# Kernel optimization log

Hardware: AMD Instinct MI355X
Metric: run time of the kernel (lower is better)

Reference implementation:

```python
import jax, jax.numpy as jnp
import numpy as np

BANDWIDTH = 1.0


def setup_inputs() -> dict:
    key = jax.random.key(0)
    k1, k2 = jax.random.split(key)
    test_data = jax.random.normal(k1, (8192, 512), dtype=jnp.float32)
    train_data = jax.random.normal(k2, (16384, 512), dtype=jnp.float32)
    return {"test_data": test_data, "train_data": train_data}


def reference(test_data, train_data):
    # test_data: [N, D], train_data: [M, D]
    bw = jnp.asarray(BANDWIDTH, dtype=test_data.dtype)
    n_train, d = train_data.shape
    # (avoids materializing the [N, M, D] difference tensor)
    x2 = jnp.sum(test_data * test_data, axis=-1, keepdims=True)        # [N, 1]
    y2 = jnp.sum(train_data * train_data, axis=-1)[None, :]           # [1, M]
    xy = jnp.einsum('nd,md->nm', test_data, train_data)               # [N, M]
    sq_dist = jnp.maximum(x2 + y2 - 2.0 * xy, 0.0)                    # [N, M]
    log_exp = -0.5 * sq_dist / (bw * bw)
    # normalization constant z = 0.5*d*log(2*pi) + d*log(bw) + log(n)
    z = (0.5 * d * jnp.log(jnp.asarray(2.0 * np.pi, dtype=test_data.dtype))
         + d * jnp.log(bw)
         + jnp.log(jnp.asarray(float(n_train), dtype=test_data.dtype)))
    return jax.scipy.special.logsumexp(log_exp - z, axis=-1)          # [N]
```

## Files before the change

kernel.cpp:

```cpp
#include <hip/hip_runtime.h>
#include <hip/hip_fp8.h>

#define D 512
#define NTEST 8192
#define NTRAIN 16384
#define BN 128
#define BM 128
#define KB 128
#define NCHUNK 8
#define NPART (NCHUNK * 2)
#define CHUNK_M (NTRAIN / NCHUNK)
#define TILES (CHUNK_M / BM)
#define ZCONST 480.20058952863157f

typedef __attribute__((ext_vector_type(4))) int int4v;
typedef __attribute__((ext_vector_type(8))) int int8v;
typedef __attribute__((ext_vector_type(4))) float floatx4;

__device__ __forceinline__ void async_copy16(const void* g, void* l) {
  __builtin_amdgcn_global_load_lds(
      (const __attribute__((address_space(1))) unsigned int*)g,
      (__attribute__((address_space(3))) unsigned int*)l, 16, 0, 0);
}

__global__ __launch_bounds__(256) void prep_kernel(
    const float* __restrict__ test, const float* __restrict__ train,
    unsigned char* __restrict__ testq, unsigned char* __restrict__ trainq,
    float* __restrict__ x2, float* __restrict__ y2) {
  const int gw = (int)((blockIdx.x * blockDim.x + threadIdx.x) >> 6);
  const int lane = threadIdx.x & 63;
  const float* src;
  unsigned char* dst;
  float* sq;
  if (gw < NTEST) {
    src = test + (size_t)gw * D;
    dst = testq + (size_t)gw * D;
    sq = x2 + gw;
  } else {
    const int r = gw - NTEST;
    src = train + (size_t)r * D;
    dst = trainq + (size_t)r * D;
    sq = y2 + r;
  }
  const int kb = lane >> 4;
  const int q = (lane >> 2) & 3;
  const int h = (lane >> 1) & 1;
  const int hb = lane & 1;
  const int sbase = kb * 128 + q * 32 + h * 16 + hb * 8;
  const int dbase = kb * 128 + h * 64 + q * 16 + hb * 8;
  float4 v0 = *(const float4*)(src + sbase);
  float4 v1 = *(const float4*)(src + sbase + 4);
  float s = v0.x * v0.x + v0.y * v0.y + v0.z * v0.z + v0.w * v0.w +
            v1.x * v1.x + v1.y * v1.y + v1.z * v1.z + v1.w * v1.w;
  float f[8] = {v0.x, v0.y, v0.z, v0.w, v1.x, v1.y, v1.z, v1.w};
  unsigned long long p = 0;
#pragma unroll
  for (int i = 0; i < 8; ++i) {
    __hip_fp8_e4m3 qv(f[i]);
    p |= (unsigned long long)qv.__x << (8 * i);
  }
  *(unsigned long long*)(dst + dbase) = p;
#pragma unroll
  for (int off = 32; off >= 1; off >>= 1) s += __shfl_xor(s, off);
  if (lane == 0) *sq = s;
}

__global__ __launch_bounds__(256, 2) void fused_kernel(
    const unsigned char* __restrict__ A, const unsigned char* __restrict__ B,
    const float* __restrict__ y2, float* __restrict__ part_m,
    float* __restrict__ part_l) {
  __shared__ unsigned char sA[BN * KB];
  __shared__ unsigned char sB[BM * KB];
  const int tid = threadIdx.x;
  const int lane = tid & 63;
  const int w = tid >> 6;
  const int lm = lane & 15;
  const int lk = lane >> 4;
  const int rowbase = blockIdx.x * BN;
  const int chunk = blockIdx.y;
  const int wrow = (w >> 1) * 64;
  const int wcol = (w & 1) * 64;

  float run_m[16], run_l[16];
#pragma unroll
  for (int i = 0; i < 16; ++i) { run_m[i] = -1e30f; run_l[i] = 0.f; }

  for (int t = 0; t < TILES; ++t) {
    const int colbase = chunk * CHUNK_M + t * BM;
    float y2v[4];
#pragma unroll
    for (int ct = 0; ct < 4; ++ct)
      y2v[ct] = y2[colbase + wcol + ct * 16 + lm];

    floatx4 acc[4][4];
#pragma unroll
    for (int rt = 0; rt < 4; ++rt)
#pragma unroll
      for (int ct = 0; ct < 4; ++ct)
        acc[rt][ct] = floatx4{0.f, 0.f, 0.f, 0.f};

    for (int kb = 0; kb < D / KB; ++kb) {
      __syncthreads();
#pragma unroll
      for (int i = 0; i < 4; ++i) {
        const int o = tid * 16 + i * 4096;
        const int r = o >> 7;
        const int csw = (o >> 4) & 7;
        const int off = ((csw ^ (r & 7)) << 4);
        async_copy16(A + (size_t)(rowbase + r) * D + kb * 128 + off, sA + o);
        async_copy16(B + (size_t)(colbase + r) * D + kb * 128 + off, sB + o);
      }
      __syncthreads();
      int8v af[4], bfr[4];
#pragma unroll
      for (int rt = 0; rt < 4; ++rt) {
        const int row = wrow + rt * 16 + lm;
        int4v lo = *(const int4v*)&sA[row * KB + ((lk ^ (row & 7)) << 4)];
        int4v hi = *(const int4v*)&sA[row * KB + (((4 + lk) ^ (row & 7)) << 4)];
        af[rt] = __builtin_shufflevector(lo, hi, 0, 1, 2, 3, 4, 5, 6, 7);
      }
#pragma unroll
      for (int ct = 0; ct < 4; ++ct) {
        const int row = wcol + ct * 16 + lm;
        int4v lo = *(const int4v*)&sB[row * KB + ((lk ^ (row & 7)) << 4)];
        int4v hi = *(const int4v*)&sB[row * KB + (((4 + lk) ^ (row & 7)) << 4)];
        bfr[ct] = __builtin_shufflevector(lo, hi, 0, 1, 2, 3, 4, 5, 6, 7);
      }
#pragma unroll
      for (int rt = 0; rt < 4; ++rt)
#pragma unroll
        for (int ct = 0; ct < 4; ++ct)
          acc[rt][ct] = __builtin_amdgcn_mfma_scale_f32_16x16x128_f8f6f4(
              af[rt], bfr[ct], acc[rt][ct], 0, 0, 0, 127, 0, 127);
    }

#pragma unroll
    for (int rt = 0; rt < 4; ++rt) {
#pragma unroll
      for (int reg = 0; reg < 4; ++reg) {
        const int idx = rt * 4 + reg;
        const float v0 = fmaf(-0.5f, y2v[0], acc[rt][0][reg]);
        const float v1 = fmaf(-0.5f, y2v[1], acc[rt][1][reg]);
        const float v2 = fmaf(-0.5f, y2v[2], acc[rt][2][reg]);
        const float v3 = fmaf(-0.5f, y2v[3], acc[rt][3][reg]);
        const float tmax = fmaxf(fmaxf(v0, v1), fmaxf(v2, v3));
        const float nm = fmaxf(run_m[idx], tmax);
        const float alpha = __expf(run_m[idx] - nm);
        const float ps = __expf(v0 - nm) + __expf(v1 - nm) +
                         __expf(v2 - nm) + __expf(v3 - nm);
        run_l[idx] = fmaf(run_l[idx], alpha, ps);
        run_m[idx] = nm;
      }
    }
  }

  const int slot = chunk * 2 + (w & 1);
#pragma unroll
  for (int rt = 0; rt < 4; ++rt) {
#pragma unroll
    for (int reg = 0; reg < 4; ++reg) {
      const int idx = rt * 4 + reg;
      float m = run_m[idx], l = run_l[idx];
#pragma unroll
      for (int off = 1; off < 16; off <<= 1) {
        const float om = __shfl_xor(m, off);
        const float ol = __shfl_xor(l, off);
        const float nm2 = fmaxf(m, om);
        l = l * __expf(m - nm2) + ol * __expf(om - nm2);
        m = nm2;
      }
      if (lm == 0) {
        const int grow = rowbase + wrow + rt * 16 + lk * 4 + reg;
        part_m[slot * NTEST + grow] = m;
        part_l[slot * NTEST + grow] = l;
      }
    }
  }
}

__global__ __launch_bounds__(256) void combine_kernel(
    const float* __restrict__ part_m, const float* __restrict__ part_l,
    const float* __restrict__ x2, float* __restrict__ out) {
  const int n = blockIdx.x * blockDim.x + threadIdx.x;
  if (n >= NTEST) return;
  float m[NPART];
  float mx = -1e30f;
#pragma unroll
  for (int c = 0; c < NPART; ++c) {
    m[c] = part_m[c * NTEST + n];
    mx = fmaxf(mx, m[c]);
  }
  float s = 0.f;
#pragma unroll
  for (int c = 0; c < NPART; ++c)
    s += part_l[c * NTEST + n] * __expf(m[c] - mx);
  out[n] = fmaf(-0.5f, x2[n], mx + __logf(s) - ZCONST);
}

extern "C" void kernel_launch(void* const* d_in, const int* in_sizes, int n_in,
                              void* d_out, int out_size, void* d_ws, size_t ws_size,
                              hipStream_t stream) {
  const float* test = (const float*)d_in[0];
  const float* train = (const float*)d_in[1];
  float* out = (float*)d_out;
  char* ws = (char*)d_ws;

  unsigned char* testq = (unsigned char*)ws;
  unsigned char* trainq = (unsigned char*)(ws + (size_t)NTEST * D);
  float* x2 = (float*)(ws + (size_t)(NTEST + NTRAIN) * D);
  float* y2 = x2 + NTEST;
  float* part_m = y2 + NTRAIN;
  float* part_l = part_m + NPART * NTEST;

  prep_kernel<<<(NTEST + NTRAIN) / 4, 256, 0, stream>>>(
      test, train, testq, trainq, x2, y2);
  fused_kernel<<<dim3(NTEST / BN, NCHUNK), 256, 0, stream>>>(
      testq, trainq, y2, part_m, part_l);
  combine_kernel<<<NTEST / 256, 256, 0, stream>>>(part_m, part_l, x2, out);
}
```

Measured before the change: 162.4 us.

## Double-buffer LDS tiles to overlap async global loads with MFMA compute

Doubles the shared-memory A/B tiles and flattens the tile and k-block loops into one round loop. Each round prefetches the next round's data into the other buffer while the current buffer is consumed by MFMAs, with a single barrier per round instead of two. The online logsumexp update and the y2 prefetch now run every fourth round. The cost is twice the LDS per block, 64 KB, which may limit how many blocks fit per CU. Overlap may also be lost if the compiler inserts a full vmcnt wait before the LDS reads.

New measurement: 184.1 us. 13.4% more time.

```diff
diff --git a/kernel.cpp b/kernel.cpp
--- a/kernel.cpp
+++ b/kernel.cpp
@@ -11,6 +11,7 @@
 #define NPART (NCHUNK * 2)
 #define CHUNK_M (NTRAIN / NCHUNK)
 #define TILES (CHUNK_M / BM)
+#define ROUNDS (TILES * (D / KB))
 #define ZCONST 480.20058952863157f
 
 typedef __attribute__((ext_vector_type(4))) int int4v;
@@ -69,8 +70,8 @@
     const unsigned char* __restrict__ A, const unsigned char* __restrict__ B,
     const float* __restrict__ y2, float* __restrict__ part_m,
     float* __restrict__ part_l) {
-  __shared__ unsigned char sA[BN * KB];
-  __shared__ unsigned char sB[BM * KB];
+  __shared__ unsigned char sA[2][BN * KB];
+  __shared__ unsigned char sB[2][BM * KB];
   const int tid = threadIdx.x;
   const int lane = tid & 63;
   const int w = tid >> 6;
@@ -81,76 +82,108 @@
   const int wrow = (w >> 1) * 64;
   const int wcol = (w & 1) * 64;
 
+  int soff[4], doff[4];
+#pragma unroll
+  for (int i = 0; i < 4; ++i) {
+    const int o = tid * 16 + i * 4096;
+    const int r = o >> 7;
+    const int csw = (o >> 4) & 7;
+    doff[i] = o;
+    soff[i] = r * D + ((csw ^ (r & 7)) << 4);
+  }
+
   float run_m[16], run_l[16];
 #pragma unroll
   for (int i = 0; i < 16; ++i) { run_m[i] = -1e30f; run_l[i] = 0.f; }
 
-  for (int t = 0; t < TILES; ++t) {
-    const int colbase = chunk * CHUNK_M + t * BM;
-    float y2v[4];
+  {
+    const int colbase0 = chunk * CHUNK_M;
+#pragma unroll
+    for (int i = 0; i < 4; ++i) {
+      async_copy16(A + (size_t)rowbase * D + soff[i], &sA[0][doff[i]]);
+      async_copy16(B + (size_t)colbase0 * D + soff[i], &sB[0][doff[i]]);
+    }
+  }
+
+  float y2v[4];
+#pragma unroll
+  for (int ct = 0; ct < 4; ++ct)
+    y2v[ct] = y2[chunk * CHUNK_M + wcol + ct * 16 + lm];
+
+  floatx4 acc[4][4];
+#pragma unroll
+  for (int rt = 0; rt < 4; ++rt)
 #pragma unroll
     for (int ct = 0; ct < 4; ++ct)
-      y2v[ct] = y2[colbase + wcol + ct * 16 + lm];
-
-    floatx4 acc[4][4];
+      acc[rt][ct] = floatx4{0.f, 0.f, 0.f, 0.f};
+
+  for (int r = 0; r < ROUNDS; ++r) {
+    const int buf = r & 1;
+    __syncthreads();
+    if (r + 1 < ROUNDS) {
+      const int rn = r + 1;
+      const int tn = rn >> 2, kbn = rn & 3;
+      const size_t abase = (size_t)rowbase * D + kbn * 128;
+      const size_t bbase = (size_t)(chunk * CHUNK_M + tn * BM) * D + kbn * 128;
+#pragma unroll
+      for (int i = 0; i < 4; ++i) {
+        async_copy16(A + abase + soff[i], &sA[buf ^ 1][doff[i]]);
+        async_copy16(B + bbase + soff[i], &sB[buf ^ 1][doff[i]]);
+      }
+    }
+
+    int8v af[4], bfr[4];
+#pragma unroll
+    for (int rt = 0; rt < 4; ++rt) {
+      const int row = wrow + rt * 16 + lm;
+      int4v lo = *(const int4v*)&sA[buf][row * KB + ((lk ^ (row & 7)) << 4)];
+      int4v hi = *(const int4v*)&sA[buf][row * KB + (((4 + lk) ^ (row & 7)) << 4)];
+      af[rt] = __builtin_shufflevector(lo, hi, 0, 1, 2, 3, 4, 5, 6, 7);
+    }
+#pragma unroll
+    for (int ct = 0; ct < 4; ++ct) {
+      const int row = wcol + ct * 16 + lm;
+      int4v lo = *(const int4v*)&sB[buf][row * KB + ((lk ^ (row & 7)) << 4)];
+      int4v hi = *(const int4v*)&sB[buf][row * KB + (((4 + lk) ^ (row & 7)) << 4)];
+      bfr[ct] = __builtin_shufflevector(lo, hi, 0, 1, 2, 3, 4, 5, 6, 7);
+    }
 #pragma unroll
     for (int rt = 0; rt < 4; ++rt)
 #pragma unroll
       for (int ct = 0; ct < 4; ++ct)
-        acc[rt][ct] = floatx4{0.f, 0.f, 0.f, 0.f};
-
-    for (int kb = 0; kb < D / KB; ++kb) {
-      __syncthreads();
-#pragma unroll
-      for (int i = 0; i < 4; ++i) {
-        const int o = tid * 16 + i * 4096;
-        const int r = o >> 7;
-        const int csw = (o >> 4) & 7;
-        const int off = ((csw ^ (r & 7)) << 4);
-        async_copy16(A + (size_t)(rowbase + r) * D + kb * 128 + off, sA + o);
-        async_copy16(B + (size_t)(colbase + r) * D + kb * 128 + off, sB + o);
-      }
-      __syncthreads();
-      int8v af[4], bfr[4];
+        acc[rt][ct] = __builtin_amdgcn_mfma_scale_f32_16x16x128_f8f6f4(
+            af[rt], bfr[ct], acc[rt][ct], 0, 0, 0, 127, 0, 127);
+
+    if ((r & 3) == 3) {
 #pragma unroll
       for (int rt = 0; rt < 4; ++rt) {
-        const int row = wrow + rt * 16 + lm;
-        int4v lo = *(const int4v*)&sA[row * KB + ((lk ^ (row & 7)) << 4)];
-        int4v hi = *(const int4v*)&sA[row * KB + (((4 + lk) ^ (row & 7)) << 4)];
-        af[rt] = __builtin_shufflevector(lo, hi, 0, 1, 2, 3, 4, 5, 6, 7);
-      }
-#pragma unroll
-      for (int ct = 0; ct < 4; ++ct) {
-        const int row = wcol + ct * 16 + lm;
-        int4v lo = *(const int4v*)&sB[row * KB + ((lk ^ (row & 7)) << 4)];
-        int4v hi = *(const int4v*)&sB[row * KB + (((4 + lk) ^ (row & 7)) << 4)];
-        bfr[ct] = __builtin_shufflevector(lo, hi, 0, 1, 2, 3, 4, 5, 6, 7);
+#pragma unroll
+        for (int reg = 0; reg < 4; ++reg) {
+          const int idx = rt * 4 + reg;
+          const float v0 = fmaf(-0.5f, y2v[0], acc[rt][0][reg]);
+          const float v1 = fmaf(-0.5f, y2v[1], acc[rt][1][reg]);
+          const float v2 = fmaf(-0.5f, y2v[2], acc[rt][2][reg]);
+          const float v3 = fmaf(-0.5f, y2v[3], acc[rt][3][reg]);
+          const float tmax = fmaxf(fmaxf(v0, v1), fmaxf(v2, v3));
+          const float nm = fmaxf(run_m[idx], tmax);
+          const float alpha = __expf(run_m[idx] - nm);
+          const float ps = __expf(v0 - nm) + __expf(v1 - nm) +
+                           __expf(v2 - nm) + __expf(v3 - nm);
+          run_l[idx] = fmaf(run_l[idx], alpha, ps);
+          run_m[idx] = nm;
+        }
+      }
+      const int tnext = (r >> 2) + 1;
+      if (tnext < TILES) {
+#pragma unroll
+        for (int ct = 0; ct < 4; ++ct)
+          y2v[ct] = y2[chunk * CHUNK_M + tnext * BM + wcol + ct * 16 + lm];
       }
 #pragma unroll
       for (int rt = 0; rt < 4; ++rt)
 #pragma unroll
         for (int ct = 0; ct < 4; ++ct)
-          acc[rt][ct] = __builtin_amdgcn_mfma_scale_f32_16x16x128_f8f6f4(
-              af[rt], bfr[ct], acc[rt][ct], 0, 0, 0, 127, 0, 127);
-    }
-
-#pragma unroll
-    for (int rt = 0; rt < 4; ++rt) {
-#pragma unroll
-      for (int reg = 0; reg < 4; ++reg) {
-        const int idx = rt * 4 + reg;
-        const float v0 = fmaf(-0.5f, y2v[0], acc[rt][0][reg]);
-        const float v1 = fmaf(-0.5f, y2v[1], acc[rt][1][reg]);
-        const float v2 = fmaf(-0.5f, y2v[2], acc[rt][2][reg]);
-        const float v3 = fmaf(-0.5f, y2v[3], acc[rt][3][reg]);
-        const float tmax = fmaxf(fmaxf(v0, v1), fmaxf(v2, v3));
-        const float nm = fmaxf(run_m[idx], tmax);
-        const float alpha = __expf(run_m[idx] - nm);
-        const float ps = __expf(v0 - nm) + __expf(v1 - nm) +
-                         __expf(v2 - nm) + __expf(v3 - nm);
-        run_l[idx] = fmaf(run_l[idx], alpha, ps);
-        run_m[idx] = nm;
-      }
+          acc[rt][ct] = floatx4{0.f, 0.f, 0.f, 0.f};
     }
   }
 
```
